# Optimization experiments

Measured on AMD Instinct MI355X. Metric: run time of the kernel, lower is better.

## Reference

```python
import jax, jax.numpy as jnp
import numpy as np

N_HEADS = 4
WINDOW = 606      # causal sliding-window width
K_PEEK = 606      # phy-output peek length (y_phy is zeros -> zeros anyway)
K_PEEK_TRUE = 30  # true-measurement peek length
LN_EPS = 1e-5


def _layernorm(x, g, b):
    m = jnp.mean(x, axis=-1, keepdims=True)
    v = jnp.var(x, axis=-1, keepdims=True)
    return (x - m) / jnp.sqrt(v + LN_EPS) * g + b


def _pos_encoding(T, d):
    pos = jnp.arange(T, dtype=jnp.float32)[:, None]
    div = jnp.exp(jnp.arange(0, d, 2, dtype=jnp.float32) * (-jnp.log(10000.0) / d))
    pe = jnp.zeros((T, d), jnp.float32)
    pe = pe.at[:, 0::2].set(jnp.sin(pos * div))
    pe = pe.at[:, 1::2].set(jnp.cos(pos * div))
    return pe


def setup_inputs() -> dict:
    key = jax.random.key(0)
    ks = iter(jax.random.split(key, 40))
    B, T, u_dim, y_dim, z_dim, h, L = 4, 2048, 8, 8, 16, 512, 4
    dff = 4 * h
    w = lambda shape: jax.random.normal(next(ks), shape, jnp.float32) * 0.02
    return {
        'u': jax.random.normal(next(ks), (B, u_dim, T), jnp.float32),
        'y': jax.random.normal(next(ks), (B, y_dim, T), jnp.float32),
        'W_in': w((u_dim + 2 * y_dim, h)), 'b_in': jnp.zeros((h,), jnp.float32),
        'qkv_w': w((L, h, 3 * h)), 'qkv_b': jnp.zeros((L, 3 * h), jnp.float32),
        'out_w': w((L, h, h)), 'out_b': jnp.zeros((L, h), jnp.float32),
        'ff1_w': w((L, h, dff)), 'ff1_b': jnp.zeros((L, dff), jnp.float32),
        'ff2_w': w((L, dff, h)), 'ff2_b': jnp.zeros((L, h), jnp.float32),
        'ln1_g': jnp.ones((L, h), jnp.float32), 'ln1_b': jnp.zeros((L, h), jnp.float32),
        'ln2_g': jnp.ones((L, h), jnp.float32), 'ln2_b': jnp.zeros((L, h), jnp.float32),
        'lnf_g': jnp.ones((h,), jnp.float32), 'lnf_b': jnp.zeros((h,), jnp.float32),
        'xm1_w': w((h, h)), 'xm1_b': jnp.zeros((h,), jnp.float32),
        'xm2_w': w((h, z_dim)), 'xm2_b': jnp.zeros((z_dim,), jnp.float32),
        'me1_w': w((z_dim, h)), 'me1_b': jnp.zeros((h,), jnp.float32),
        'me2_w': w((h, h)), 'me2_b': jnp.zeros((h,), jnp.float32),
        'me3_w': w((h, y_dim)), 'me3_b': jnp.zeros((y_dim,), jnp.float32),
    }


def _forward(u, y, W_in, b_in, qkv_w, qkv_b, out_w, out_b, ff1_w, ff1_b,
             ff2_w, ff2_b, ln1_g, ln1_b, ln2_g, ln2_b, lnf_g, lnf_b,
             xm1_w, xm1_b, xm2_w, xm2_b, me1_w, me1_b, me2_w, me2_b, me3_w, me3_b):
    B, y_dim, T = y.shape
    u_t = jnp.transpose(u, (0, 2, 1))          # [B,T,u_dim]
    y_t = jnp.transpose(y, (0, 2, 1))          # [B,T,y_dim]
    # phy rollout produces zeros (zero-init MODEL_PHY surrogate) -> y_aug = 0
    y_aug = jnp.zeros((B, T, y_dim), jnp.float32)
    k_true = min(K_PEEK_TRUE, T)
    y_aug_true = jnp.concatenate(
        [y_t[:, :k_true, :], jnp.zeros((B, T - k_true, y_dim), jnp.float32)], axis=1)
    u_aug = jnp.concatenate([u_t, y_aug, y_aug_true], axis=2)  # [B,T,u+2y]

    h = W_in.shape[1]
    x = u_aug @ W_in + b_in + _pos_encoding(T, h)[None]        # [B,T,h]

    # causal sliding-window mask: row i attends to j in [i-WINDOW+1, i]
    i = jnp.arange(T)[:, None]
    j = jnp.arange(T)[None, :]
    allowed = (j <= i) & (j > i - WINDOW)                      # [T,T] bool

    dh = h // N_HEADS
    L = qkv_w.shape[0]
    for l in range(L):
        qkv = x @ qkv_w[l] + qkv_b[l]                          # [B,T,3h]
        q, k, v = jnp.split(qkv, 3, axis=-1)
        q = q.reshape(B, T, N_HEADS, dh)
        k = k.reshape(B, T, N_HEADS, dh)
        v = v.reshape(B, T, N_HEADS, dh)
        scores = jnp.einsum('bqhd,bkhd->bhqk', q, k) / jnp.sqrt(jnp.float32(dh))
        scores = jnp.where(allowed[None, None], scores, jnp.float32(-1e30))
        probs = jax.nn.softmax(scores, axis=-1)
        attn = jnp.einsum('bhqk,bkhd->bqhd', probs, v).reshape(B, T, h)
        attn = attn @ out_w[l] + out_b[l]
        x = _layernorm(x + attn, ln1_g[l], ln1_b[l])           # post-norm
        ff = jax.nn.gelu(x @ ff1_w[l] + ff1_b[l], approximate=False) @ ff2_w[l] + ff2_b[l]
        x = _layernorm(x + ff, ln2_g[l], ln2_b[l])
    x = _layernorm(x, lnf_g, lnf_b)

    x_mean = jax.nn.gelu(x @ xm1_w + xm1_b, approximate=False) @ xm2_w + xm2_b
    hme = jax.nn.gelu(x_mean @ me1_w + me1_b, approximate=False)
    hme = jax.nn.gelu(hme @ me2_w + me2_b, approximate=False)
    y_hat = hme @ me3_w + me3_b                                # [B,T,y_dim]

    loss = jnp.sum((y_hat - y_t) ** 2)                         # lamba_smooth = 0
    return loss


def reference(u, y, W_in, b_in, qkv_w, qkv_b, out_w, out_b, ff1_w, ff1_b,
              ff2_w, ff2_b, ln1_g, ln1_b, ln2_g, ln2_b, lnf_g, lnf_b,
              xm1_w, xm1_b, xm2_w, xm2_b, me1_w, me1_b, me2_w, me2_b, me3_w, me3_b):
    return _forward(u, y, W_in, b_in, qkv_w, qkv_b, out_w, out_b, ff1_w, ff1_b,
                    ff2_w, ff2_b, ln1_g, ln1_b, ln2_g, ln2_b, lnf_g, lnf_b,
                    xm1_w, xm1_b, xm2_w, xm2_b, me1_w, me1_b, me2_w, me2_b, me3_w, me3_b)
```

## Files before the change

kernel.cpp:

```cpp
#include <hip/hip_runtime.h>
#include <cstdint>
#include <cstddef>

#define TT 2048
#define BB 4
#define HDIM 512
#define NH 4
#define LAYERS 4
#define WINDOW 606

#define PLANE_QK 4194304ull
#define PLANE_X  4194304ull
#define PLANE_FF 16777216ull

typedef __attribute__((ext_vector_type(8))) short bf16x8s;
typedef __attribute__((ext_vector_type(4))) float f32x4;

__device__ __forceinline__ float wred_sum(float v) {
#pragma unroll
  for (int off = 32; off; off >>= 1) v += __shfl_xor(v, off, 64);
  return v;
}
__device__ __forceinline__ float gelu_exact(float x) {
  return 0.5f * x * (1.0f + erff(x * 0.70710678118654752f));
}
__device__ __forceinline__ ushort bf16_rne(float v) {
  uint32_t u = __float_as_uint(v);
  u += 0x7FFFu + ((u >> 16) & 1u);
  return (ushort)(u >> 16);
}
__device__ __forceinline__ void split3(float v, ushort& h, ushort& l) {
  h = bf16_rne(v);
  const float hf = __uint_as_float(((uint32_t)h) << 16);
  l = bf16_rne(v - hf);
}
__device__ __forceinline__ void gld_lds16(const void* g, void* l) {
  __builtin_amdgcn_global_load_lds(
      (const __attribute__((address_space(1))) uint32_t*)g,
      (__attribute__((address_space(3))) uint32_t*)l, 16, 0, 0);
}

__global__ __launch_bounds__(256) void embed_kernel(
    const float* __restrict__ u, const float* __restrict__ y,
    const float* __restrict__ W_in, const float* __restrict__ b_in,
    float* __restrict__ X, ushort* __restrict__ xp) {
  const int row = blockIdx.x;
  const int b = row >> 11;
  const int t = row & 2047;
  const int tid = threadIdx.x;
  __shared__ float ua[24];
  if (tid < 8)       ua[tid] = u[((b << 3) + tid) * TT + t];
  else if (tid < 16) ua[tid] = 0.0f;
  else if (tid < 24) ua[tid] = (t < 30) ? y[((b << 3) + (tid - 16)) * TT + t] : 0.0f;
  __syncthreads();
#pragma unroll
  for (int c0 = 0; c0 < 2; ++c0) {
    const int c = c0 * 256 + tid;
    float s = b_in[c];
#pragma unroll
    for (int k = 0; k < 24; ++k) s += ua[k] * W_in[k * HDIM + c];
    const float dv = expf(-0.0179889460337f * (float)(c & ~1));
    const float arg = (float)t * dv;
    s += (c & 1) ? cosf(arg) : sinf(arg);
    X[(size_t)row * HDIM + c] = s;
    ushort h, l2; split3(s, h, l2);
    xp[(size_t)row * HDIM + c] = h;
    xp[PLANE_X + (size_t)row * HDIM + c] = l2;
  }
}

__device__ __forceinline__ void pack_tile(float (*tile)[33],
    const float* __restrict__ W, ushort* __restrict__ Wp,
    int K, int N, int bk, int bn, int tid) {
  const int i0 = tid >> 5, j = tid & 31;
#pragma unroll
  for (int i = 0; i < 4; ++i) {
    const int kk = i0 + i * 8;
    tile[kk][j] = W[(size_t)(bk + kk) * N + bn + j];
  }
  __syncthreads();
  const size_t NK = (size_t)N * K;
#pragma unroll
  for (int i = 0; i < 4; ++i) {
    const int nn = i0 + i * 8;
    const float v = tile[j][nn];
    ushort h, l2; split3(v, h, l2);
    ushort* base = Wp + (size_t)(bn + nn) * K + bk + j;
    base[0] = h; base[NK] = l2;
  }
}

__global__ __launch_bounds__(256) void packL_kernel(
    const float* __restrict__ qkvw, const float* __restrict__ outw,
    const float* __restrict__ ff1w, ushort* __restrict__ Wp) {
  __shared__ float tile[32][33];
  int i = blockIdx.x;
  if (i < 768) {
    pack_tile(tile, qkvw, Wp, 512, 1536, (i & 15) * 32, (i >> 4) * 32, threadIdx.x);
  } else if (i < 1024) {
    i -= 768;
    pack_tile(tile, outw, Wp + 1572864, 512, 512, (i & 15) * 32, (i >> 4) * 32, threadIdx.x);
  } else {
    i -= 1024;
    pack_tile(tile, ff1w, Wp + 2097152, 512, 2048, (i & 15) * 32, (i >> 4) * 32, threadIdx.x);
  }
}

__global__ __launch_bounds__(256) void packF_kernel(
    const float* __restrict__ ff2w, ushort* __restrict__ Wp) {
  __shared__ float tile[32][33];
  const int i = blockIdx.x;
  pack_tile(tile, ff2w, Wp, 2048, 512, (i & 63) * 32, (i >> 6) * 32, threadIdx.x);
}

__global__ __launch_bounds__(256) void packH_kernel(
    const float* __restrict__ xm1w, const float* __restrict__ me2w,
    ushort* __restrict__ Wp) {
  __shared__ float tile[32][33];
  int i = blockIdx.x;
  if (i < 256) pack_tile(tile, xm1w, Wp, 512, 512, (i & 15) * 32, (i >> 4) * 32, threadIdx.x);
  else { i -= 256; pack_tile(tile, me2w, Wp + 524288, 512, 512, (i & 15) * 32, (i >> 4) * 32, threadIdx.x); }
}

template <int ACT, int OUTMODE, int RM>
__global__ __launch_bounds__(256) void gemm_mfma(
    const ushort* __restrict__ Ah, const ushort* __restrict__ Al,
    const ushort* __restrict__ Bh, const ushort* __restrict__ Bl,
    const float* __restrict__ bias,
    float* __restrict__ C, ushort* __restrict__ Cp, size_t cplane,
    ushort* __restrict__ Wq, int M, int N, int K) {
  constexpr int IA = RM / 32;
  constexpr int JA = RM / 64;
  __shared__ ushort Als[RM * 32];
  __shared__ ushort Bls[4096];
  __shared__ float biasL[128];
  const int tid = threadIdx.x;
  const int bn = blockIdx.x * 128, bm = blockIdx.y * RM;
  const int w = tid >> 6, ln = tid & 63;
  const int wr = (w >> 1) * (RM / 2), wc = (w & 1) * 64;
  const int c = ln & 15, g = ln >> 4;
  if (tid < 128) biasL[tid] = bias[bn + tid];

  const int srow = tid >> 2;
  const int scol = (tid & 3) * 8;

  f32x4 acc[IA][4] = {};
#pragma unroll
  for (int term = 0; term < 3; ++term) {
    const ushort* Ag = (term == 1) ? Al : Ah;
    const ushort* Bg = (term == 2) ? Bl : Bh;
    for (int k0 = 0; k0 < K; k0 += 32) {
#pragma unroll
      for (int j = 0; j < JA; ++j) {
        const int off = j * 4096 + tid * 16;
        gld_lds16(Ag + (size_t)(bm + j * 64 + srow) * K + k0 + scol, (char*)Als + off);
      }
#pragma unroll
      for (int j = 0; j < 2; ++j) {
        const int off = j * 4096 + tid * 16;
        gld_lds16(Bg + (size_t)(bn + j * 64 + srow) * K + k0 + scol, (char*)Bls + off);
      }
      __syncthreads();
      bf16x8s fa[IA], fb[4];
#pragma unroll
      for (int i = 0; i < IA; ++i)
        fa[i] = *(const bf16x8s*)&Als[(wr + i * 16 + c) * 32 + g * 8];
#pragma unroll
      for (int i = 0; i < 4; ++i)
        fb[i] = *(const bf16x8s*)&Bls[(wc + i * 16 + c) * 32 + g * 8];
#pragma unroll
      for (int i = 0; i < IA; ++i)
#pragma unroll
        for (int j = 0; j < 4; ++j)
          acc[i][j] = __builtin_amdgcn_mfma_f32_16x16x32_bf16(fa[i], fb[j], acc[i][j], 0, 0, 0);
      __syncthreads();
    }
  }
  const float qscale = 0.08838834764831845f * 1.44269504088896341f;
#pragma unroll
  for (int i = 0; i < IA; ++i) {
    const int grow0 = bm + wr + i * 16 + g * 4;
#pragma unroll
    for (int j = 0; j < 4; ++j) {
      const int gcol = bn + wc + j * 16 + c;
      const float bv = biasL[wc + j * 16 + c];
      if (OUTMODE == 2) {
        const int bq = grow0 >> 11, tl = grow0 & 2047;
        if (bn < 512) {
          const int hh = gcol >> 7, d = gcol & 127;
          ushort* dst = Wq + ((size_t)(bq * NH + hh) * TT + tl) * 128 + d;
#pragma unroll
          for (int r = 0; r < 4; ++r) {
            ushort h, l2; split3((acc[i][j][r] + bv) * qscale, h, l2);
            dst[(size_t)r * 128] = h;
            dst[PLANE_QK + (size_t)r * 128] = l2;
          }
        } else if (bn < 1024) {
          const int hh = (gcol - 512) >> 7, d = gcol & 127;
          ushort* dst = Wq + 2 * PLANE_QK + ((size_t)(bq * NH + hh) * TT + tl) * 128 + d;
#pragma unroll
          for (int r = 0; r < 4; ++r) {
            ushort h, l2; split3(acc[i][j][r] + bv, h, l2);
            dst[(size_t)r * 128] = h;
            dst[PLANE_QK + (size_t)r * 128] = l2;
          }
        } else {
          const int hh = (gcol - 1024) >> 7, d = gcol & 127;
          ushort4 h4, l4;
          split3(acc[i][j][0] + bv, h4.x, l4.x);
          split3(acc[i][j][1] + bv, h4.y, l4.y);
          split3(acc[i][j][2] + bv, h4.z, l4.z);
          split3(acc[i][j][3] + bv, h4.w, l4.w);
          ushort* dst = Wq + 4 * PLANE_QK + ((size_t)(bq * NH + hh) * 128 + d) * TT + tl;
          *(ushort4*)dst = h4;
          *(ushort4*)(dst + PLANE_QK) = l4;
        }
      } else {
#pragma unroll
        for (int r = 0; r < 4; ++r) {
          float v = acc[i][j][r] + bv;
          if (ACT) v = gelu_exact(v);
          if (OUTMODE == 1) {
            ushort h, l2; split3(v, h, l2);
            ushort* base = Cp + (size_t)(grow0 + r) * N + gcol;
            base[0] = h; base[cplane] = l2;
          } else {
            C[(size_t)(grow0 + r) * N + gcol] = v;
          }
        }
      }
    }
  }
}

template <int ACT, int PACK>
__global__ __launch_bounds__(256) void gemm_bias(
    const float* __restrict__ A, const float* __restrict__ B,
    const float* __restrict__ bias, float* __restrict__ C,
    ushort* __restrict__ Cp, size_t cplane, int M, int N, int K) {
  __shared__ float As[16][132];
  __shared__ float Bs[16][64];
  const int bm = blockIdx.y * 128;
  const int bn = blockIdx.x * 64;
  const int tid = threadIdx.x;
  const int tx = tid & 15, ty = tid >> 4;
  float acc[8][4] = {};
  for (int k0 = 0; k0 < K; k0 += 16) {
#pragma unroll
    for (int i = 0; i < 8; ++i) {
      const int idx = i * 256 + tid;
      const int m = idx >> 4, k = idx & 15;
      As[k][m] = A[(size_t)(bm + m) * K + k0 + k];
    }
#pragma unroll
    for (int i = 0; i < 4; ++i) {
      const int idx = i * 256 + tid;
      const int k = idx >> 6, n = idx & 63;
      Bs[k][n] = (bn + n < N) ? B[(size_t)(k0 + k) * N + bn + n] : 0.0f;
    }
    __syncthreads();
#pragma unroll
    for (int kk = 0; kk < 16; ++kk) {
      float a[8], bb[4];
#pragma unroll
      for (int i = 0; i < 8; ++i) a[i] = As[kk][ty * 8 + i];
#pragma unroll
      for (int j = 0; j < 4; ++j) bb[j] = Bs[kk][tx * 4 + j];
#pragma unroll
      for (int i = 0; i < 8; ++i)
#pragma unroll
        for (int j = 0; j < 4; ++j) acc[i][j] += a[i] * bb[j];
    }
    __syncthreads();
  }
#pragma unroll
  for (int i = 0; i < 8; ++i) {
    const int m = bm + ty * 8 + i;
#pragma unroll
    for (int j = 0; j < 4; ++j) {
      const int n = bn + tx * 4 + j;
      if (n < N) {
        float v = acc[i][j] + bias[n];
        if (ACT) v = gelu_exact(v);
        if (PACK) {
          ushort h, l2; split3(v, h, l2);
          ushort* base = Cp + (size_t)m * N + n;
          base[0] = h; base[cplane] = l2;
        } else {
          C[(size_t)m * N + n] = v;
        }
      }
    }
  }
}

__global__ __launch_bounds__(256) void attn_mfma(
    const ushort* __restrict__ QKVp, ushort* __restrict__ atp) {
  const int bid = blockIdx.x;
  const int lid = (bid & 7) * 128 + (bid >> 3);
  const int q0 = (lid & 63) * 32;
  const int bh = lid >> 6;
  const int b = bh >> 2, hh = bh & 3;
  const int tid = threadIdx.x;
  const int w = tid >> 6, lane = tid & 63;
  const int c = lane & 15, g = lane >> 4;
  const int wr = w >> 1, wc = w & 1;

  __shared__ ushort Ph[32][40], Pl[32][40];
  __shared__ float wmax[2][32], wsum[2][32];
  __shared__ float mrow[2][32], lrow[2][32];

  const ushort* Qh = QKVp;
  const ushort* Ql = QKVp + PLANE_QK;
  const ushort* Kh = QKVp + 2 * PLANE_QK;
  const ushort* Kl = QKVp + 3 * PLANE_QK;
  const ushort* Vh = QKVp + 4 * PLANE_QK;
  const ushort* Vl = QKVp + 5 * PLANE_QK;

  const size_t qkbase = (size_t)bh * TT * 128;
  const size_t vtbase = (size_t)bh * 128 * TT;

  bf16x8s qh[4], ql[4];
  {
    const ushort* qr = Qh + qkbase + (size_t)(q0 + wr * 16 + c) * 128 + g * 8;
    const ushort* qr2 = Ql + qkbase + (size_t)(q0 + wr * 16 + c) * 128 + g * 8;
#pragma unroll
    for (int kc = 0; kc < 4; ++kc) {
      qh[kc] = *(const bf16x8s*)(qr + kc * 32);
      ql[kc] = *(const bf16x8s*)(qr2 + kc * 32);
    }
  }

  if (tid < 32) { mrow[0][tid] = -1e30f; lrow[0][tid] = 0.0f; }
  __syncthreads();

  f32x4 oacc[2][2] = {};
  int par = 0;
  int lo_ = q0 - (WINDOW - 1); if (lo_ < 0) lo_ = 0;
  const int k_first = lo_ & ~31;
  const int qg = q0 + wr * 16 + c;
  const int qrow = wr * 16 + c;

  for (int k0 = k_first; k0 <= q0; k0 += 32) {
    const bf16x8s vh0 = *(const bf16x8s*)(Vh + vtbase + (size_t)(w * 32 + c) * TT + k0 + g * 8);
    const bf16x8s vh1 = *(const bf16x8s*)(Vh + vtbase + (size_t)(w * 32 + 16 + c) * TT + k0 + g * 8);
    const bf16x8s vl0 = *(const bf16x8s*)(Vl + vtbase + (size_t)(w * 32 + c) * TT + k0 + g * 8);
    const bf16x8s vl1 = *(const bf16x8s*)(Vl + vtbase + (size_t)(w * 32 + 16 + c) * TT + k0 + g * 8);

    f32x4 sacc = {};
    {
      const ushort* kr = Kh + qkbase + (size_t)(k0 + wc * 16 + c) * 128 + g * 8;
      const ushort* kr2 = Kl + qkbase + (size_t)(k0 + wc * 16 + c) * 128 + g * 8;
      bf16x8s kh[4], kl[4];
#pragma unroll
      for (int kc = 0; kc < 4; ++kc) {
        kh[kc] = *(const bf16x8s*)(kr + kc * 32);
        kl[kc] = *(const bf16x8s*)(kr2 + kc * 32);
      }
#pragma unroll
      for (int kc = 0; kc < 4; ++kc)
        sacc = __builtin_amdgcn_mfma_f32_16x16x32_bf16(kh[kc], qh[kc], sacc, 0, 0, 0);
#pragma unroll
      for (int kc = 0; kc < 4; ++kc)
        sacc = __builtin_amdgcn_mfma_f32_16x16x32_bf16(kl[kc], qh[kc], sacc, 0, 0, 0);
#pragma unroll
      for (int kc = 0; kc < 4; ++kc)
        sacc = __builtin_amdgcn_mfma_f32_16x16x32_bf16(kh[kc], ql[kc], sacc, 0, 0, 0);
    }
    float s[4];
    float m4 = -1e30f;
#pragma unroll
    for (int r = 0; r < 4; ++r) {
      const int kj = k0 + wc * 16 + g * 4 + r;
      const bool ok = (kj <= qg) && (kj > qg - WINDOW);
      s[r] = ok ? sacc[r] : -1e30f;
      m4 = fmaxf(m4, s[r]);
    }
    m4 = fmaxf(m4, __shfl_xor(m4, 16, 64));
    m4 = fmaxf(m4, __shfl_xor(m4, 32, 64));
    if (lane < 16) wmax[wc][qrow] = m4;
    __syncthreads();

    {
      const float mt = fmaxf(wmax[0][qrow], wmax[1][qrow]);
      const float mn = fmaxf(mrow[par][qrow], mt);
      float pv[4];
      float ps = 0.0f;
#pragma unroll
      for (int r = 0; r < 4; ++r) {
        pv[r] = (s[r] > -1e29f) ? exp2f(s[r] - mn) : 0.0f;
        ps += pv[r];
      }
      ps += __shfl_xor(ps, 16, 64);
      ps += __shfl_xor(ps, 32, 64);
      if (lane < 16) wsum[wc][qrow] = ps;
      ushort4 h4, l4;
      split3(pv[0], h4.x, l4.x); split3(pv[1], h4.y, l4.y);
      split3(pv[2], h4.z, l4.z); split3(pv[3], h4.w, l4.w);
      *(ushort4*)&Ph[qrow][wc * 16 + g * 4] = h4;
      *(ushort4*)&Pl[qrow][wc * 16 + g * 4] = l4;
    }
    __syncthreads();

    if (tid < 32) {
      const float mt = fmaxf(wmax[0][tid], wmax[1][tid]);
      const float mo = mrow[par][tid];
      const float mn = fmaxf(mo, mt);
      mrow[par ^ 1][tid] = mn;
      lrow[par ^ 1][tid] = lrow[par][tid] * exp2f(mo - mn) + wsum[0][tid] + wsum[1][tid];
    }
#pragma unroll
    for (int rh = 0; rh < 2; ++rh) {
      float sc[4];
#pragma unroll
      for (int r = 0; r < 4; ++r) {
        const int row = rh * 16 + g * 4 + r;
        const float mt = fmaxf(wmax[0][row], wmax[1][row]);
        const float mo = mrow[par][row];
        sc[r] = exp2f(mo - fmaxf(mo, mt));
      }
#pragma unroll
      for (int jt = 0; jt < 2; ++jt)
#pragma unroll
        for (int r = 0; r < 4; ++r) oacc[rh][jt][r] *= sc[r];
      const bf16x8s pah = *(const bf16x8s*)&Ph[rh * 16 + c][g * 8];
      const bf16x8s pal = *(const bf16x8s*)&Pl[rh * 16 + c][g * 8];
      oacc[rh][0] = __builtin_amdgcn_mfma_f32_16x16x32_bf16(pah, vh0, oacc[rh][0], 0, 0, 0);
      oacc[rh][0] = __builtin_amdgcn_mfma_f32_16x16x32_bf16(pal, vh0, oacc[rh][0], 0, 0, 0);
      oacc[rh][0] = __builtin_amdgcn_mfma_f32_16x16x32_bf16(pah, vl0, oacc[rh][0], 0, 0, 0);
      oacc[rh][1] = __builtin_amdgcn_mfma_f32_16x16x32_bf16(pah, vh1, oacc[rh][1], 0, 0, 0);
      oacc[rh][1] = __builtin_amdgcn_mfma_f32_16x16x32_bf16(pal, vh1, oacc[rh][1], 0, 0, 0);
      oacc[rh][1] = __builtin_amdgcn_mfma_f32_16x16x32_bf16(pah, vl1, oacc[rh][1], 0, 0, 0);
    }
    __syncthreads();
    par ^= 1;
  }

#pragma unroll
  for (int rh = 0; rh < 2; ++rh) {
#pragma unroll
    for (int r = 0; r < 4; ++r) {
      const int row = rh * 16 + g * 4 + r;
      const float li = 1.0f / lrow[par][row];
      const int qgo = q0 + row;
      ushort* base = atp + (size_t)(b * TT + qgo) * HDIM + hh * 128;
#pragma unroll
      for (int jt = 0; jt < 2; ++jt) {
        const int d = w * 32 + jt * 16 + c;
        ushort h, l2; split3(oacc[rh][jt][r] * li, h, l2);
        base[d] = h;
        base[PLANE_X + d] = l2;
      }
    }
  }
}

template <int HAS_RES>
__global__ __launch_bounds__(128) void ln_kernel(
    const float* __restrict__ x, const float* __restrict__ r,
    const float* __restrict__ g, const float* __restrict__ be,
    float* __restrict__ out, ushort* __restrict__ xp) {
  const int row = blockIdx.x, tid = threadIdx.x;
  float4 v = ((const float4*)(x + (size_t)row * HDIM))[tid];
  if (HAS_RES) {
    const float4 rv = ((const float4*)(r + (size_t)row * HDIM))[tid];
    v.x += rv.x; v.y += rv.y; v.z += rv.z; v.w += rv.w;
  }
  __shared__ float red[2];
  float s = v.x + v.y + v.z + v.w;
  s = wred_sum(s);
  if ((tid & 63) == 0) red[tid >> 6] = s;
  __syncthreads();
  const float mean = (red[0] + red[1]) * (1.0f / 512.0f);
  const float dx = v.x - mean, dy = v.y - mean, dz = v.z - mean, dw = v.w - mean;
  float s2 = dx * dx + dy * dy + dz * dz + dw * dw;
  __syncthreads();
  s2 = wred_sum(s2);
  if ((tid & 63) == 0) red[tid >> 6] = s2;
  __syncthreads();
  const float var = (red[0] + red[1]) * (1.0f / 512.0f);
  const float inv = 1.0f / sqrtf(var + 1e-5f);
  const float4 gv = ((const float4*)g)[tid];
  const float4 bv = ((const float4*)be)[tid];
  float4 o;
  o.x = dx * inv * gv.x + bv.x;
  o.y = dy * inv * gv.y + bv.y;
  o.z = dz * inv * gv.z + bv.z;
  o.w = dw * inv * gv.w + bv.w;
  ((float4*)(out + (size_t)row * HDIM))[tid] = o;
  ushort4 h4, l4;
  split3(o.x, h4.x, l4.x); split3(o.y, h4.y, l4.y);
  split3(o.z, h4.z, l4.z); split3(o.w, h4.w, l4.w);
  ushort* basep = xp + (size_t)row * HDIM + tid * 4;
  *(ushort4*)basep = h4;
  *(ushort4*)(basep + PLANE_X) = l4;
}

__global__ __launch_bounds__(256) void head_loss_kernel(
    const float* __restrict__ hme, const float* __restrict__ w3,
    const float* __restrict__ b3, const float* __restrict__ y,
    float* __restrict__ partials) {
  const int row = blockIdx.x;
  const int b = row >> 11, t = row & 2047;
  const int tid = threadIdx.x;
  __shared__ __align__(16) float hl[512];
  __shared__ float acc8[8];
  ((float2*)hl)[tid] = ((const float2*)(hme + (size_t)row * HDIM))[tid];
  __syncthreads();
  const int d = tid >> 5, l32 = tid & 31;
  float s = 0.0f;
  for (int k = l32; k < 512; k += 32) s += hl[k] * w3[k * 8 + d];
#pragma unroll
  for (int off = 16; off; off >>= 1) s += __shfl_xor(s, off, 64);
  if (l32 == 0) {
    const float yh = s + b3[d];
    const float diff = yh - y[((b << 3) + d) * TT + t];
    acc8[d] = diff * diff;
  }
  __syncthreads();
  if (tid == 0) {
    float tot = 0.0f;
#pragma unroll
    for (int i = 0; i < 8; ++i) tot += acc8[i];
    partials[row] = tot;
  }
}

__global__ __launch_bounds__(256) void reduce_kernel(
    const float* __restrict__ partials, float* __restrict__ out, int n) {
  float s = 0.0f;
  for (int i = threadIdx.x; i < n; i += 256) s += partials[i];
  s = wred_sum(s);
  __shared__ float red[4];
  if ((threadIdx.x & 63) == 0) red[threadIdx.x >> 6] = s;
  __syncthreads();
  if (threadIdx.x == 0) out[0] = red[0] + red[1] + red[2] + red[3];
}

extern "C" void kernel_launch(void* const* d_in, const int* in_sizes, int n_in,
                              void* d_out, int out_size, void* d_ws, size_t ws_size,
                              hipStream_t stream) {
  (void)in_sizes; (void)n_in; (void)out_size; (void)ws_size;
  const float* u     = (const float*)d_in[0];
  const float* y     = (const float*)d_in[1];
  const float* W_in  = (const float*)d_in[2];
  const float* b_in  = (const float*)d_in[3];
  const float* qkv_w = (const float*)d_in[4];
  const float* qkv_b = (const float*)d_in[5];
  const float* out_w = (const float*)d_in[6];
  const float* out_b = (const float*)d_in[7];
  const float* ff1_w = (const float*)d_in[8];
  const float* ff1_b = (const float*)d_in[9];
  const float* ff2_w = (const float*)d_in[10];
  const float* ff2_b = (const float*)d_in[11];
  const float* ln1_g = (const float*)d_in[12];
  const float* ln1_b = (const float*)d_in[13];
  const float* ln2_g = (const float*)d_in[14];
  const float* ln2_b = (const float*)d_in[15];
  const float* lnf_g = (const float*)d_in[16];
  const float* lnf_b = (const float*)d_in[17];
  const float* xm1_w = (const float*)d_in[18];
  const float* xm1_b = (const float*)d_in[19];
  const float* xm2_w = (const float*)d_in[20];
  const float* xm2_b = (const float*)d_in[21];
  const float* me1_w = (const float*)d_in[22];
  const float* me1_b = (const float*)d_in[23];
  const float* me2_w = (const float*)d_in[24];
  const float* me2_b = (const float*)d_in[25];
  const float* me3_w = (const float*)d_in[26];
  const float* me3_b = (const float*)d_in[27];

  const int M = BB * TT;
  char* ws = (char*)d_ws;
  float*  X    = (float*)(ws);
  float*  PRJ  = (float*)(ws + ((size_t)16 << 20));
  ushort* BIGp = (ushort*)(ws + ((size_t)32 << 20));
  ushort* PK1  = (ushort*)(ws + ((size_t)96 << 20));
  ushort* WSCR = (ushort*)(ws + ((size_t)112 << 20));
  float*  XM   = (float*)(ws + ((size_t)120 << 20));
  float*  PART = (float*)(ws + ((size_t)121 << 20));

  embed_kernel<<<M, 256, 0, stream>>>(u, y, W_in, b_in, X, PK1);

  for (int l = 0; l < LAYERS; ++l) {
    packL_kernel<<<2048, 256, 0, stream>>>(
        qkv_w + (size_t)l * 512 * 1536, out_w + (size_t)l * 512 * 512,
        ff1_w + (size_t)l * 512 * 2048, WSCR);
    gemm_mfma<0, 2, 128><<<dim3(12, 64), 256, 0, stream>>>(
        PK1, PK1 + PLANE_X, WSCR, WSCR + 786432, qkv_b + l * 1536,
        nullptr, nullptr, 0, BIGp, M, 1536, 512);
    attn_mfma<<<1024, 256, 0, stream>>>(BIGp, PK1);
    gemm_mfma<0, 0, 64><<<dim3(4, 128), 256, 0, stream>>>(
        PK1, PK1 + PLANE_X, WSCR + 1572864, WSCR + 1835008, out_b + l * 512,
        PRJ, nullptr, 0, nullptr, M, 512, 512);
    ln_kernel<1><<<M, 128, 0, stream>>>(X, PRJ, ln1_g + l * 512, ln1_b + l * 512, X, PK1);
    gemm_mfma<1, 1, 128><<<dim3(16, 64), 256, 0, stream>>>(
        PK1, PK1 + PLANE_X, WSCR + 2097152, WSCR + 3145728, ff1_b + l * 2048,
        nullptr, BIGp, PLANE_FF, nullptr, M, 2048, 512);
    packF_kernel<<<1024, 256, 0, stream>>>(ff2_w + (size_t)l * 2048 * 512, WSCR);
    gemm_mfma<0, 0, 64><<<dim3(4, 128), 256, 0, stream>>>(
        BIGp, BIGp + PLANE_FF, WSCR, WSCR + 1048576, ff2_b + l * 512,
        PRJ, nullptr, 0, nullptr, M, 512, 2048);
    ln_kernel<1><<<M, 128, 0, stream>>>(X, PRJ, ln2_g + l * 512, ln2_b + l * 512, X, PK1);
  }
  ln_kernel<0><<<M, 128, 0, stream>>>(X, nullptr, lnf_g, lnf_b, X, PK1);

  packH_kernel<<<512, 256, 0, stream>>>(xm1_w, me2_w, WSCR);
  gemm_mfma<1, 0, 64><<<dim3(4, 128), 256, 0, stream>>>(
      PK1, PK1 + PLANE_X, WSCR, WSCR + 262144, xm1_b,
      PRJ, nullptr, 0, nullptr, M, 512, 512);
  gemm_bias<0, 0><<<dim3(1, 64), 256, 0, stream>>>(PRJ, xm2_w, xm2_b, XM, nullptr, 0, M, 16, 512);
  gemm_bias<1, 1><<<dim3(8, 64), 256, 0, stream>>>(XM, me1_w, me1_b, nullptr, PK1, PLANE_X, M, 512, 16);
  gemm_mfma<1, 0, 64><<<dim3(4, 128), 256, 0, stream>>>(
      PK1, PK1 + PLANE_X, WSCR + 524288, WSCR + 786432, me2_b,
      PRJ, nullptr, 0, nullptr, M, 512, 512);
  head_loss_kernel<<<M, 256, 0, stream>>>(PRJ, me3_w, me3_b, y, PART);
  reduce_kernel<<<1, 256, 0, stream>>>(PART, (float*)d_out, M);
}
```

Baseline: 2.147 ms.

## Restructure attention so each wave owns 16 query rows with register softmax

The attention kernel is rewritten so each wave handles an independent 16-row query tile across the whole head dimension. The online-softmax max and sum now live in registers, and the P matrix is rebuilt into an MFMA operand with lane shuffles, which removes the shared-memory staging and the three block-wide barriers per key step. Each block now covers 64 queries and the grid is halved. In exchange each wave loads all of K and V for its keys, so V traffic per wave grows, and register pressure rises with 8 output accumulators.

```diff
diff --git a/kernel.cpp b/kernel.cpp
--- a/kernel.cpp
+++ b/kernel.cpp
@@ -294,21 +294,37 @@
   }
 }
 
+__device__ __forceinline__ void bfrag_from_pairs(
+    uint32_t P0, uint32_t P1, uint32_t P2, uint32_t P3,
+    int c, int g, uint32_t w[4]) {
+  const int s0 = c + 16 * ((2 * g) & 3);
+  const int s1 = c + 16 * ((2 * g + 1) & 3);
+  const uint32_t a0 = (uint32_t)__shfl((int)P0, s0, 64);
+  const uint32_t b0 = (uint32_t)__shfl((int)P2, s0, 64);
+  const uint32_t a1 = (uint32_t)__shfl((int)P1, s0, 64);
+  const uint32_t b1 = (uint32_t)__shfl((int)P3, s0, 64);
+  const uint32_t a2 = (uint32_t)__shfl((int)P0, s1, 64);
+  const uint32_t b2 = (uint32_t)__shfl((int)P2, s1, 64);
+  const uint32_t a3 = (uint32_t)__shfl((int)P1, s1, 64);
+  const uint32_t b3 = (uint32_t)__shfl((int)P3, s1, 64);
+  const bool lo = (g < 2);
+  w[0] = lo ? a0 : b0;
+  w[1] = lo ? a1 : b1;
+  w[2] = lo ? a2 : b2;
+  w[3] = lo ? a3 : b3;
+}
+
 __global__ __launch_bounds__(256) void attn_mfma(
     const ushort* __restrict__ QKVp, ushort* __restrict__ atp) {
   const int bid = blockIdx.x;
-  const int lid = (bid & 7) * 128 + (bid >> 3);
-  const int q0 = (lid & 63) * 32;
-  const int bh = lid >> 6;
+  const int lid = (bid & 7) * 64 + (bid >> 3);
+  const int qb = lid & 31;
+  const int bh = lid >> 5;
   const int b = bh >> 2, hh = bh & 3;
   const int tid = threadIdx.x;
   const int w = tid >> 6, lane = tid & 63;
   const int c = lane & 15, g = lane >> 4;
-  const int wr = w >> 1, wc = w & 1;
-
-  __shared__ ushort Ph[32][40], Pl[32][40];
-  __shared__ float wmax[2][32], wsum[2][32];
-  __shared__ float mrow[2][32], lrow[2][32];
+  const int q0w = qb * 64 + w * 16;
 
   const ushort* Qh = QKVp;
   const ushort* Ql = QKVp + PLANE_QK;
@@ -316,142 +332,129 @@
   const ushort* Kl = QKVp + 3 * PLANE_QK;
   const ushort* Vh = QKVp + 4 * PLANE_QK;
   const ushort* Vl = QKVp + 5 * PLANE_QK;
-
   const size_t qkbase = (size_t)bh * TT * 128;
   const size_t vtbase = (size_t)bh * 128 * TT;
 
-  bf16x8s qh[4], ql[4];
+  bf16x8s qfh[4], qfl[4];
   {
-    const ushort* qr = Qh + qkbase + (size_t)(q0 + wr * 16 + c) * 128 + g * 8;
-    const ushort* qr2 = Ql + qkbase + (size_t)(q0 + wr * 16 + c) * 128 + g * 8;
+    const ushort* qr  = Qh + qkbase + (size_t)(q0w + c) * 128 + g * 8;
+    const ushort* qr2 = Ql + qkbase + (size_t)(q0w + c) * 128 + g * 8;
 #pragma unroll
     for (int kc = 0; kc < 4; ++kc) {
-      qh[kc] = *(const bf16x8s*)(qr + kc * 32);
-      ql[kc] = *(const bf16x8s*)(qr2 + kc * 32);
-    }
-  }
-
-  if (tid < 32) { mrow[0][tid] = -1e30f; lrow[0][tid] = 0.0f; }
-  __syncthreads();
-
-  f32x4 oacc[2][2] = {};
-  int par = 0;
-  int lo_ = q0 - (WINDOW - 1); if (lo_ < 0) lo_ = 0;
+      qfh[kc] = *(const bf16x8s*)(qr + kc * 32);
+      qfl[kc] = *(const bf16x8s*)(qr2 + kc * 32);
+    }
+  }
+
+  float m_reg = -1e30f, l_reg = 0.0f;
+  f32x4 oacc[8] = {};
+
+  int lo_ = q0w - (WINDOW - 1); if (lo_ < 0) lo_ = 0;
   const int k_first = lo_ & ~31;
-  const int qg = q0 + wr * 16 + c;
-  const int qrow = wr * 16 + c;
-
-  for (int k0 = k_first; k0 <= q0; k0 += 32) {
-    const bf16x8s vh0 = *(const bf16x8s*)(Vh + vtbase + (size_t)(w * 32 + c) * TT + k0 + g * 8);
-    const bf16x8s vh1 = *(const bf16x8s*)(Vh + vtbase + (size_t)(w * 32 + 16 + c) * TT + k0 + g * 8);
-    const bf16x8s vl0 = *(const bf16x8s*)(Vl + vtbase + (size_t)(w * 32 + c) * TT + k0 + g * 8);
-    const bf16x8s vl1 = *(const bf16x8s*)(Vl + vtbase + (size_t)(w * 32 + 16 + c) * TT + k0 + g * 8);
-
-    f32x4 sacc = {};
+  const int k_last = (q0w + 15) & ~31;
+  const int qg = q0w + c;
+
+  for (int k0 = k_first; k0 <= k_last; k0 += 32) {
+    f32x4 s0 = {}, s1 = {};
     {
-      const ushort* kr = Kh + qkbase + (size_t)(k0 + wc * 16 + c) * 128 + g * 8;
-      const ushort* kr2 = Kl + qkbase + (size_t)(k0 + wc * 16 + c) * 128 + g * 8;
-      bf16x8s kh[4], kl[4];
+      const ushort* k0h = Kh + qkbase + (size_t)(k0 + c) * 128 + g * 8;
+      const ushort* k1h = Kh + qkbase + (size_t)(k0 + 16 + c) * 128 + g * 8;
+      const ushort* k0l = Kl + qkbase + (size_t)(k0 + c) * 128 + g * 8;
+      const ushort* k1l = Kl + qkbase + (size_t)(k0 + 16 + c) * 128 + g * 8;
+      bf16x8s kf0h[4], kf1h[4], kf0l[4], kf1l[4];
 #pragma unroll
       for (int kc = 0; kc < 4; ++kc) {
-        kh[kc] = *(const bf16x8s*)(kr + kc * 32);
-        kl[kc] = *(const bf16x8s*)(kr2 + kc * 32);
-      }
-#pragma unroll
-      for (int kc = 0; kc < 4; ++kc)
-        sacc = __builtin_amdgcn_mfma_f32_16x16x32_bf16(kh[kc], qh[kc], sacc, 0, 0, 0);
-#pragma unroll
-      for (int kc = 0; kc < 4; ++kc)
-        sacc = __builtin_amdgcn_mfma_f32_16x16x32_bf16(kl[kc], qh[kc], sacc, 0, 0, 0);
-#pragma unroll
-      for (int kc = 0; kc < 4; ++kc)
-        sacc = __builtin_amdgcn_mfma_f32_16x16x32_bf16(kh[kc], ql[kc], sacc, 0, 0, 0);
-    }
-    float s[4];
-    float m4 = -1e30f;
+        kf0h[kc] = *(const bf16x8s*)(k0h + kc * 32);
+        kf1h[kc] = *(const bf16x8s*)(k1h + kc * 32);
+        kf0l[kc] = *(const bf16x8s*)(k0l + kc * 32);
+        kf1l[kc] = *(const bf16x8s*)(k1l + kc * 32);
+      }
+#pragma unroll
+      for (int kc = 0; kc < 4; ++kc) {
+        s0 = __builtin_amdgcn_mfma_f32_16x16x32_bf16(kf0h[kc], qfh[kc], s0, 0, 0, 0);
+        s1 = __builtin_amdgcn_mfma_f32_16x16x32_bf16(kf1h[kc], qfh[kc], s1, 0, 0, 0);
+      }
+#pragma unroll
+      for (int kc = 0; kc < 4; ++kc) {
+        s0 = __builtin_amdgcn_mfma_f32_16x16x32_bf16(kf0l[kc], qfh[kc], s0, 0, 0, 0);
+        s1 = __builtin_amdgcn_mfma_f32_16x16x32_bf16(kf1l[kc], qfh[kc], s1, 0, 0, 0);
+      }
+#pragma unroll
+      for (int kc = 0; kc < 4; ++kc) {
+        s0 = __builtin_amdgcn_mfma_f32_16x16x32_bf16(kf0h[kc], qfl[kc], s0, 0, 0, 0);
+        s1 = __builtin_amdgcn_mfma_f32_16x16x32_bf16(kf1h[kc], qfl[kc], s1, 0, 0, 0);
+      }
+    }
+    float e[8];
+    float mx = -1e30f;
 #pragma unroll
     for (int r = 0; r < 4; ++r) {
-      const int kj = k0 + wc * 16 + g * 4 + r;
-      const bool ok = (kj <= qg) && (kj > qg - WINDOW);
-      s[r] = ok ? sacc[r] : -1e30f;
-      m4 = fmaxf(m4, s[r]);
-    }
-    m4 = fmaxf(m4, __shfl_xor(m4, 16, 64));
-    m4 = fmaxf(m4, __shfl_xor(m4, 32, 64));
-    if (lane < 16) wmax[wc][qrow] = m4;
-    __syncthreads();
-
-    {
-      const float mt = fmaxf(wmax[0][qrow], wmax[1][qrow]);
-      const float mn = fmaxf(mrow[par][qrow], mt);
-      float pv[4];
-      float ps = 0.0f;
-#pragma unroll
-      for (int r = 0; r < 4; ++r) {
-        pv[r] = (s[r] > -1e29f) ? exp2f(s[r] - mn) : 0.0f;
-        ps += pv[r];
-      }
-      ps += __shfl_xor(ps, 16, 64);
-      ps += __shfl_xor(ps, 32, 64);
-      if (lane < 16) wsum[wc][qrow] = ps;
-      ushort4 h4, l4;
-      split3(pv[0], h4.x, l4.x); split3(pv[1], h4.y, l4.y);
-      split3(pv[2], h4.z, l4.z); split3(pv[3], h4.w, l4.w);
-      *(ushort4*)&Ph[qrow][wc * 16 + g * 4] = h4;
-      *(ushort4*)&Pl[qrow][wc * 16 + g * 4] = l4;
-    }
-    __syncthreads();
-
-    if (tid < 32) {
-      const float mt = fmaxf(wmax[0][tid], wmax[1][tid]);
-      const float mo = mrow[par][tid];
-      const float mn = fmaxf(mo, mt);
-      mrow[par ^ 1][tid] = mn;
-      lrow[par ^ 1][tid] = lrow[par][tid] * exp2f(mo - mn) + wsum[0][tid] + wsum[1][tid];
-    }
-#pragma unroll
-    for (int rh = 0; rh < 2; ++rh) {
-      float sc[4];
-#pragma unroll
-      for (int r = 0; r < 4; ++r) {
-        const int row = rh * 16 + g * 4 + r;
-        const float mt = fmaxf(wmax[0][row], wmax[1][row]);
-        const float mo = mrow[par][row];
-        sc[r] = exp2f(mo - fmaxf(mo, mt));
-      }
-#pragma unroll
-      for (int jt = 0; jt < 2; ++jt)
-#pragma unroll
-        for (int r = 0; r < 4; ++r) oacc[rh][jt][r] *= sc[r];
-      const bf16x8s pah = *(const bf16x8s*)&Ph[rh * 16 + c][g * 8];
-      const bf16x8s pal = *(const bf16x8s*)&Pl[rh * 16 + c][g * 8];
-      oacc[rh][0] = __builtin_amdgcn_mfma_f32_16x16x32_bf16(pah, vh0, oacc[rh][0], 0, 0, 0);
-      oacc[rh][0] = __builtin_amdgcn_mfma_f32_16x16x32_bf16(pal, vh0, oacc[rh][0], 0, 0, 0);
-      oacc[rh][0] = __builtin_amdgcn_mfma_f32_16x16x32_bf16(pah, vl0, oacc[rh][0], 0, 0, 0);
-      oacc[rh][1] = __builtin_amdgcn_mfma_f32_16x16x32_bf16(pah, vh1, oacc[rh][1], 0, 0, 0);
-      oacc[rh][1] = __builtin_amdgcn_mfma_f32_16x16x32_bf16(pal, vh1, oacc[rh][1], 0, 0, 0);
-      oacc[rh][1] = __builtin_amdgcn_mfma_f32_16x16x32_bf16(pah, vl1, oacc[rh][1], 0, 0, 0);
-    }
-    __syncthreads();
-    par ^= 1;
-  }
-
-#pragma unroll
-  for (int rh = 0; rh < 2; ++rh) {
-#pragma unroll
-    for (int r = 0; r < 4; ++r) {
-      const int row = rh * 16 + g * 4 + r;
-      const float li = 1.0f / lrow[par][row];
-      const int qgo = q0 + row;
-      ushort* base = atp + (size_t)(b * TT + qgo) * HDIM + hh * 128;
-#pragma unroll
-      for (int jt = 0; jt < 2; ++jt) {
-        const int d = w * 32 + jt * 16 + c;
-        ushort h, l2; split3(oacc[rh][jt][r] * li, h, l2);
-        base[d] = h;
-        base[PLANE_X + d] = l2;
-      }
-    }
+      const int kj0 = k0 + 4 * g + r;
+      const int kj1 = kj0 + 16;
+      const bool ok0 = (kj0 <= qg) && (kj0 > qg - WINDOW);
+      const bool ok1 = (kj1 <= qg) && (kj1 > qg - WINDOW);
+      e[r]     = ok0 ? s0[r] : -1e30f;
+      e[4 + r] = ok1 ? s1[r] : -1e30f;
+      mx = fmaxf(mx, fmaxf(e[r], e[4 + r]));
+    }
+    mx = fmaxf(mx, __shfl_xor(mx, 16, 64));
+    mx = fmaxf(mx, __shfl_xor(mx, 32, 64));
+    const float mn = fmaxf(m_reg, mx);
+    const float rescale = exp2f(m_reg - mn);
+    float ps = 0.0f;
+#pragma unroll
+    for (int i = 0; i < 8; ++i) {
+      e[i] = (e[i] > -1e29f) ? exp2f(e[i] - mn) : 0.0f;
+      ps += e[i];
+    }
+    ps += __shfl_xor(ps, 16, 64);
+    ps += __shfl_xor(ps, 32, 64);
+    l_reg = l_reg * rescale + ps;
+    m_reg = mn;
+#pragma unroll
+    for (int i = 0; i < 8; ++i)
+#pragma unroll
+      for (int r = 0; r < 4; ++r) oacc[i][r] *= rescale;
+
+    ushort hh8[8], ll8[8];
+#pragma unroll
+    for (int i = 0; i < 8; ++i) split3(e[i], hh8[i], ll8[i]);
+    const uint32_t P0h = (uint32_t)hh8[0] | ((uint32_t)hh8[1] << 16);
+    const uint32_t P1h = (uint32_t)hh8[2] | ((uint32_t)hh8[3] << 16);
+    const uint32_t P2h = (uint32_t)hh8[4] | ((uint32_t)hh8[5] << 16);
+    const uint32_t P3h = (uint32_t)hh8[6] | ((uint32_t)hh8[7] << 16);
+    const uint32_t P0l = (uint32_t)ll8[0] | ((uint32_t)ll8[1] << 16);
+    const uint32_t P1l = (uint32_t)ll8[2] | ((uint32_t)ll8[3] << 16);
+    const uint32_t P2l = (uint32_t)ll8[4] | ((uint32_t)ll8[5] << 16);
+    const uint32_t P3l = (uint32_t)ll8[6] | ((uint32_t)ll8[7] << 16);
+    union { uint32_t u[4]; bf16x8s v; } ph, pl;
+    bfrag_from_pairs(P0h, P1h, P2h, P3h, c, g, ph.u);
+    bfrag_from_pairs(P0l, P1l, P2l, P3l, c, g, pl.u);
+
+#pragma unroll
+    for (int i = 0; i < 8; ++i) {
+      const ushort* va = Vh + vtbase + (size_t)(i * 16 + c) * TT + k0 + g * 8;
+      const ushort* vb = Vl + vtbase + (size_t)(i * 16 + c) * TT + k0 + g * 8;
+      const bf16x8s vfh = *(const bf16x8s*)va;
+      const bf16x8s vfl = *(const bf16x8s*)vb;
+      oacc[i] = __builtin_amdgcn_mfma_f32_16x16x32_bf16(vfh, ph.v, oacc[i], 0, 0, 0);
+      oacc[i] = __builtin_amdgcn_mfma_f32_16x16x32_bf16(vfh, pl.v, oacc[i], 0, 0, 0);
+      oacc[i] = __builtin_amdgcn_mfma_f32_16x16x32_bf16(vfl, ph.v, oacc[i], 0, 0, 0);
+    }
+  }
+
+  const float li = 1.0f / l_reg;
+  ushort* rowbase = atp + (size_t)(b * TT + q0w + c) * HDIM + hh * 128;
+#pragma unroll
+  for (int i = 0; i < 8; ++i) {
+    ushort4 h4, l4;
+    split3(oacc[i][0] * li, h4.x, l4.x);
+    split3(oacc[i][1] * li, h4.y, l4.y);
+    split3(oacc[i][2] * li, h4.z, l4.z);
+    split3(oacc[i][3] * li, h4.w, l4.w);
+    ushort* dst = rowbase + i * 16 + 4 * g;
+    *(ushort4*)dst = h4;
+    *(ushort4*)(dst + PLANE_X) = l4;
   }
 }
 
@@ -589,7 +592,7 @@
     gemm_mfma<0, 2, 128><<<dim3(12, 64), 256, 0, stream>>>(
         PK1, PK1 + PLANE_X, WSCR, WSCR + 786432, qkv_b + l * 1536,
         nullptr, nullptr, 0, BIGp, M, 1536, 512);
-    attn_mfma<<<1024, 256, 0, stream>>>(BIGp, PK1);
+    attn_mfma<<<512, 256, 0, stream>>>(BIGp, PK1);
     gemm_mfma<0, 0, 64><<<dim3(4, 128), 256, 0, stream>>>(
         PK1, PK1 + PLANE_X, WSCR + 1572864, WSCR + 1835008, out_b + l * 512,
         PRJ, nullptr, 0, nullptr, M, 512, 512);
```

Result: slower. 2.278 ms (+6.1%).

## Fuse split-bf16 GEMM terms into one K-loop and remap blocks for XCD locality

Applied to the files above, without the earlier changes.

The three-pass split-precision GEMM (hi*hi, lo*hi, hi*lo) now runs as a single K loop that loads the hi and lo tiles of both A and B into LDS together and issues all three MFMAs per fragment pair. This removes the repeated global reads of A and B tiles across passes and cuts the number of K-loop barriers. It also switches to a 1D grid with a blockIdx remap so that consecutive logical tiles land on the same XCD, which should improve L2 reuse. The cost is doubled LDS use per block, which may reduce occupancy.

```diff
diff --git a/kernel.cpp b/kernel.cpp
--- a/kernel.cpp
+++ b/kernel.cpp
@@ -128,53 +128,66 @@
     const ushort* __restrict__ Bh, const ushort* __restrict__ Bl,
     const float* __restrict__ bias,
     float* __restrict__ C, ushort* __restrict__ Cp, size_t cplane,
-    ushort* __restrict__ Wq, int M, int N, int K) {
+    ushort* __restrict__ Wq, int M, int N, int K, int nbn) {
   constexpr int IA = RM / 32;
   constexpr int JA = RM / 64;
-  __shared__ ushort Als[RM * 32];
-  __shared__ ushort Bls[4096];
+  __shared__ ushort AlsH[RM * 32];
+  __shared__ ushort AlsL[RM * 32];
+  __shared__ ushort BlsH[4096];
+  __shared__ ushort BlsL[4096];
   __shared__ float biasL[128];
   const int tid = threadIdx.x;
-  const int bn = blockIdx.x * 128, bm = blockIdx.y * RM;
+  const int cpx = (int)gridDim.x >> 3;
+  const int bid = blockIdx.x;
+  const int lid = (bid & 7) * cpx + (bid >> 3);
+  const int bn = (lid % nbn) * 128;
+  const int bm = (lid / nbn) * RM;
   const int w = tid >> 6, ln = tid & 63;
   const int wr = (w >> 1) * (RM / 2), wc = (w & 1) * 64;
   const int c = ln & 15, g = ln >> 4;
   if (tid < 128) biasL[tid] = bias[bn + tid];
-
   const int srow = tid >> 2;
   const int scol = (tid & 3) * 8;
 
   f32x4 acc[IA][4] = {};
-#pragma unroll
-  for (int term = 0; term < 3; ++term) {
-    const ushort* Ag = (term == 1) ? Al : Ah;
-    const ushort* Bg = (term == 2) ? Bl : Bh;
-    for (int k0 = 0; k0 < K; k0 += 32) {
-#pragma unroll
-      for (int j = 0; j < JA; ++j) {
-        const int off = j * 4096 + tid * 16;
-        gld_lds16(Ag + (size_t)(bm + j * 64 + srow) * K + k0 + scol, (char*)Als + off);
+  for (int k0 = 0; k0 < K; k0 += 32) {
+#pragma unroll
+    for (int j = 0; j < JA; ++j) {
+      const size_t ga = (size_t)(bm + j * 64 + srow) * K + k0 + scol;
+      const int off = j * 4096 + tid * 16;
+      gld_lds16(Ah + ga, (char*)AlsH + off);
+      gld_lds16(Al + ga, (char*)AlsL + off);
+    }
+#pragma unroll
+    for (int j = 0; j < 2; ++j) {
+      const size_t gb = (size_t)(bn + j * 64 + srow) * K + k0 + scol;
+      const int off = j * 4096 + tid * 16;
+      gld_lds16(Bh + gb, (char*)BlsH + off);
+      gld_lds16(Bl + gb, (char*)BlsL + off);
+    }
+    __syncthreads();
+    bf16x8s fah[IA], fal[IA], fbh[4], fbl[4];
+#pragma unroll
+    for (int i = 0; i < IA; ++i) {
+      const int ao = (wr + i * 16 + c) * 32 + g * 8;
+      fah[i] = *(const bf16x8s*)&AlsH[ao];
+      fal[i] = *(const bf16x8s*)&AlsL[ao];
+    }
+#pragma unroll
+    for (int i = 0; i < 4; ++i) {
+      const int bo = (wc + i * 16 + c) * 32 + g * 8;
+      fbh[i] = *(const bf16x8s*)&BlsH[bo];
+      fbl[i] = *(const bf16x8s*)&BlsL[bo];
+    }
+#pragma unroll
+    for (int i = 0; i < IA; ++i)
+#pragma unroll
+      for (int j = 0; j < 4; ++j) {
+        acc[i][j] = __builtin_amdgcn_mfma_f32_16x16x32_bf16(fah[i], fbh[j], acc[i][j], 0, 0, 0);
+        acc[i][j] = __builtin_amdgcn_mfma_f32_16x16x32_bf16(fal[i], fbh[j], acc[i][j], 0, 0, 0);
+        acc[i][j] = __builtin_amdgcn_mfma_f32_16x16x32_bf16(fah[i], fbl[j], acc[i][j], 0, 0, 0);
       }
-#pragma unroll
-      for (int j = 0; j < 2; ++j) {
-        const int off = j * 4096 + tid * 16;
-        gld_lds16(Bg + (size_t)(bn + j * 64 + srow) * K + k0 + scol, (char*)Bls + off);
-      }
-      __syncthreads();
-      bf16x8s fa[IA], fb[4];
-#pragma unroll
-      for (int i = 0; i < IA; ++i)
-        fa[i] = *(const bf16x8s*)&Als[(wr + i * 16 + c) * 32 + g * 8];
-#pragma unroll
-      for (int i = 0; i < 4; ++i)
-        fb[i] = *(const bf16x8s*)&Bls[(wc + i * 16 + c) * 32 + g * 8];
-#pragma unroll
-      for (int i = 0; i < IA; ++i)
-#pragma unroll
-        for (int j = 0; j < 4; ++j)
-          acc[i][j] = __builtin_amdgcn_mfma_f32_16x16x32_bf16(fa[i], fb[j], acc[i][j], 0, 0, 0);
-      __syncthreads();
-    }
+    __syncthreads();
   }
   const float qscale = 0.08838834764831845f * 1.44269504088896341f;
 #pragma unroll
@@ -586,34 +599,34 @@
     packL_kernel<<<2048, 256, 0, stream>>>(
         qkv_w + (size_t)l * 512 * 1536, out_w + (size_t)l * 512 * 512,
         ff1_w + (size_t)l * 512 * 2048, WSCR);
-    gemm_mfma<0, 2, 128><<<dim3(12, 64), 256, 0, stream>>>(
+    gemm_mfma<0, 2, 128><<<768, 256, 0, stream>>>(
         PK1, PK1 + PLANE_X, WSCR, WSCR + 786432, qkv_b + l * 1536,
-        nullptr, nullptr, 0, BIGp, M, 1536, 512);
+        nullptr, nullptr, 0, BIGp, M, 1536, 512, 12);
     attn_mfma<<<1024, 256, 0, stream>>>(BIGp, PK1);
-    gemm_mfma<0, 0, 64><<<dim3(4, 128), 256, 0, stream>>>(
+    gemm_mfma<0, 0, 64><<<512, 256, 0, stream>>>(
         PK1, PK1 + PLANE_X, WSCR + 1572864, WSCR + 1835008, out_b + l * 512,
-        PRJ, nullptr, 0, nullptr, M, 512, 512);
+        PRJ, nullptr, 0, nullptr, M, 512, 512, 4);
     ln_kernel<1><<<M, 128, 0, stream>>>(X, PRJ, ln1_g + l * 512, ln1_b + l * 512, X, PK1);
-    gemm_mfma<1, 1, 128><<<dim3(16, 64), 256, 0, stream>>>(
+    gemm_mfma<1, 1, 128><<<1024, 256, 0, stream>>>(
         PK1, PK1 + PLANE_X, WSCR + 2097152, WSCR + 3145728, ff1_b + l * 2048,
-        nullptr, BIGp, PLANE_FF, nullptr, M, 2048, 512);
+        nullptr, BIGp, PLANE_FF, nullptr, M, 2048, 512, 16);
     packF_kernel<<<1024, 256, 0, stream>>>(ff2_w + (size_t)l * 2048 * 512, WSCR);
-    gemm_mfma<0, 0, 64><<<dim3(4, 128), 256, 0, stream>>>(
+    gemm_mfma<0, 0, 64><<<512, 256, 0, stream>>>(
         BIGp, BIGp + PLANE_FF, WSCR, WSCR + 1048576, ff2_b + l * 512,
-        PRJ, nullptr, 0, nullptr, M, 512, 2048);
+        PRJ, nullptr, 0, nullptr, M, 512, 2048, 4);
     ln_kernel<1><<<M, 128, 0, stream>>>(X, PRJ, ln2_g + l * 512, ln2_b + l * 512, X, PK1);
   }
   ln_kernel<0><<<M, 128, 0, stream>>>(X, nullptr, lnf_g, lnf_b, X, PK1);
 
   packH_kernel<<<512, 256, 0, stream>>>(xm1_w, me2_w, WSCR);
-  gemm_mfma<1, 0, 64><<<dim3(4, 128), 256, 0, stream>>>(
+  gemm_mfma<1, 0, 64><<<512, 256, 0, stream>>>(
       PK1, PK1 + PLANE_X, WSCR, WSCR + 262144, xm1_b,
-      PRJ, nullptr, 0, nullptr, M, 512, 512);
+      PRJ, nullptr, 0, nullptr, M, 512, 512, 4);
   gemm_bias<0, 0><<<dim3(1, 64), 256, 0, stream>>>(PRJ, xm2_w, xm2_b, XM, nullptr, 0, M, 16, 512);
   gemm_bias<1, 1><<<dim3(8, 64), 256, 0, stream>>>(XM, me1_w, me1_b, nullptr, PK1, PLANE_X, M, 512, 16);
-  gemm_mfma<1, 0, 64><<<dim3(4, 128), 256, 0, stream>>>(
+  gemm_mfma<1, 0, 64><<<512, 256, 0, stream>>>(
       PK1, PK1 + PLANE_X, WSCR + 524288, WSCR + 786432, me2_b,
-      PRJ, nullptr, 0, nullptr, M, 512, 512);
+      PRJ, nullptr, 0, nullptr, M, 512, 512, 4);
   head_loss_kernel<<<M, 256, 0, stream>>>(PRJ, me3_w, me3_b, y, PART);
   reduce_kernel<<<1, 256, 0, stream>>>(PART, (float*)d_out, M);
 }
```

Result: faster. 1.854 ms (-13.6%).
